# Performance work log

Hardware: AMD Instinct MI355X
Metric: run time of the kernel (lower is better)

## Reference

```python
import jax, jax.numpy as jnp
import numpy as np

B, N, D = 4, 1024, 512
H = 8
HD = D // H  # 64
EPS = 1e-12  # F.normalize eps


def _l2_normalize(t):
    # torch.nn.functional.normalize(p=2, dim=-1): x / max(||x||_2, eps)
    nrm = jnp.sqrt(jnp.sum(t * t, axis=-1, keepdims=True))
    return t / jnp.maximum(nrm, EPS)


def setup_inputs() -> dict:
    key = jax.random.key(0)
    ks = jax.random.split(key, 5)
    scale = 1.0 / np.sqrt(D)
    inp = {
        "x": jax.random.normal(ks[0], (B, N, D), dtype=jnp.float32),
        "Wq": jax.random.normal(ks[1], (D, D), dtype=jnp.float32) * scale,
        "Wk": jax.random.normal(ks[2], (D, D), dtype=jnp.float32) * scale,
        "Wv": jax.random.normal(ks[3], (D, D), dtype=jnp.float32) * scale,
        "Wo": jax.random.normal(ks[4], (D, D), dtype=jnp.float32) * scale,
        "bq": jnp.zeros((D,), dtype=jnp.float32),
        "bk": jnp.zeros((D,), dtype=jnp.float32),
        "bv": jnp.zeros((D,), dtype=jnp.float32),
        "bo": jnp.zeros((D,), dtype=jnp.float32),
    }
    return inp


def reference(x, Wq, Wk, Wv, Wo, bq, bk, bv, bo):
    b, n, d = x.shape
    # projections (nn.Linear: x @ W.T + b), split heads -> (b, h, n, hd)
    def split_heads(t):
        return t.reshape(b, n, H, HD).transpose(0, 2, 1, 3)

    q = split_heads(x @ Wq.T + bq)
    k = split_heads(x @ Wk.T + bk)
    v = split_heads(x @ Wv.T + bv)

    q = _l2_normalize(jax.nn.elu(q))
    k = _l2_normalize(jax.nn.elu(k))

    # causal linear attention: running prefix sum of k (outer) v states
    kv_step = jnp.einsum('bhnd,bhne->bhnde', k, v)      # (b,h,n,hd,hd)
    kv_prefix = jnp.cumsum(kv_step, axis=2)             # causal prefix state
    out = jnp.einsum('bhnd,bhnde->bhne', q, kv_prefix)  # (b,h,n,hd)

    out = out.transpose(0, 2, 1, 3).reshape(b, n, d)
    return out @ Wo.T + bo
```

## Files before the change

kernel.cpp:

```cpp
#include <hip/hip_runtime.h>
#include <cmath>

#define BB 4
#define NN 1024
#define DD 512
#define HH 8
#define HDIM 64
#define ROWS (BB * NN)
#define NCHUNK 16
#define KA 512
#define WMAT ((size_t)512 * 512)

typedef _Float16 f16;
typedef f16   f16x8 __attribute__((ext_vector_type(8)));
typedef f16   f16x4 __attribute__((ext_vector_type(4)));
typedef float f32x4 __attribute__((ext_vector_type(4)));

#define GLOAD_LDS16(g, l) \
    __builtin_amdgcn_global_load_lds((const __attribute__((address_space(1))) void*)(g), \
                                     (__attribute__((address_space(3))) void*)(l), 16, 0, 0)

__global__ __launch_bounds__(256)
void split_all(const float* __restrict__ x,
               const float* __restrict__ Wq, const float* __restrict__ Wk,
               const float* __restrict__ Wv, const float* __restrict__ Wo,
               f16* __restrict__ xa, f16* __restrict__ wa)
{
    const int bid = blockIdx.x;
    const float* src;
    f16* dstbase;
    int t;
    if (bid < 2048) {
        t = bid * 256 + threadIdx.x;
        src = x;
        dstbase = xa;
    } else {
        int wb = bid - 2048;
        int m  = wb >> 8;
        t = (wb & 255) * 256 + threadIdx.x;
        src = (m == 0) ? Wq : (m == 1) ? Wk : (m == 2) ? Wv : Wo;
        dstbase = wa + (size_t)m * WMAT;
    }
    float4 v = ((const float4*)src)[t];
    int r = t >> 7;
    int c = (t & 127) * 4;
    f16x4 h;
    h[0] = (f16)v.x; h[1] = (f16)v.y; h[2] = (f16)v.z; h[3] = (f16)v.w;
    *(f16x4*)(dstbase + (size_t)r * 512 + c) = h;
}

template<int OUTMODE>
__global__ __launch_bounds__(256)
void mm_f16(const f16* __restrict__ A, const f16* __restrict__ Wm,
            const float* __restrict__ b0, const float* __restrict__ b1,
            const float* __restrict__ b2,
            f16* __restrict__ qf, f16* __restrict__ kf,
            f16* __restrict__ ktb, f16* __restrict__ vtb,
            float* __restrict__ obase)
{
    constexpr int BN = (OUTMODE == 0) ? 128 : 64;
    constexpr int NW = BN / 32;
    constexpr int BR = BN / 32;

    __shared__ __align__(16) f16 As[128 * 64];
    __shared__ __align__(16) f16 Bs[BN * 64];

    const int t    = threadIdx.x;
    const int lane = t & 63;
    const int wid  = t >> 6;
    const int wr   = wid >> 1;
    const int wc   = wid & 1;
    const int l16  = lane & 15;
    const int g16  = lane >> 4;

    const int nwg = 32 * gridDim.y;
    const int lin = blockIdx.y * 32 + blockIdx.x;
    const int swz = (lin & 7) * (nwg >> 3) + (lin >> 3);
    const int bx  = swz & 31;
    const int by  = swz >> 5;

    const int r0 = bx * 128;
    const int c0 = by * BN;
    const int z  = (OUTMODE == 0) ? (c0 >> 9) : 0;
    const int cw = (OUTMODE == 0) ? (c0 & 511) : c0;

    const f16* Wz = Wm + (size_t)z * WMAT;

    f32x4 acc[4][NW] = {};

    for (int kt = 0; kt < 8; ++kt) {
        const int kb = kt * 64;
        #pragma unroll
        for (int i = 0; i < 4; ++i) {
            int f = i * 256 + t;
            int row = f >> 3;
            int sc  = (f & 7) ^ (row & 7);
            GLOAD_LDS16(A + (size_t)(r0 + row) * KA + kb + sc * 8, As + f * 8);
        }
        #pragma unroll
        for (int i = 0; i < BR; ++i) {
            int f = i * 256 + t;
            int row = f >> 3;
            int sc  = (f & 7) ^ (row & 7);
            GLOAD_LDS16(Wz + (size_t)(cw + row) * KA + kb + sc * 8, Bs + f * 8);
        }
        __syncthreads();

        #pragma unroll
        for (int kk = 0; kk < 2; ++kk) {
            f16x8 af[4], bfr[NW];
            #pragma unroll
            for (int mi = 0; mi < 4; ++mi) {
                int lr = wr * 64 + mi * 16 + l16;
                int sc = (kk * 4 + g16) ^ (lr & 7);
                af[mi] = *(const f16x8*)(As + lr * 64 + sc * 8);
            }
            #pragma unroll
            for (int ni = 0; ni < NW; ++ni) {
                int lr = wc * (BN / 2) + ni * 16 + l16;
                int sc = (kk * 4 + g16) ^ (lr & 7);
                bfr[ni] = *(const f16x8*)(Bs + lr * 64 + sc * 8);
            }
            #pragma unroll
            for (int mi = 0; mi < 4; ++mi)
                #pragma unroll
                for (int ni = 0; ni < NW; ++ni)
                    acc[mi][ni] = __builtin_amdgcn_mfma_f32_16x16x32_f16(af[mi], bfr[ni], acc[mi][ni], 0, 0, 0);
        }
        __syncthreads();
    }

    if (OUTMODE == 1) {
        #pragma unroll
        for (int mi = 0; mi < 4; ++mi)
            #pragma unroll
            for (int ni = 0; ni < NW; ++ni) {
                int cg = c0 + wc * (BN / 2) + ni * 16 + l16;
                float bv = b0[cg];
                #pragma unroll
                for (int r = 0; r < 4; ++r) {
                    int rg = r0 + wr * 64 + mi * 16 + g16 * 4 + r;
                    obase[(size_t)rg * DD + cg] = acc[mi][ni][r] + bv;
                }
            }
    } else {
        const float* bias = (z == 0) ? b0 : (z == 1) ? b1 : b2;

        #pragma unroll
        for (int mi = 0; mi < 4; ++mi)
            #pragma unroll
            for (int ni = 0; ni < NW; ++ni) {
                float bv = bias[cw + wc * 64 + ni * 16 + l16];
                #pragma unroll
                for (int r = 0; r < 4; ++r) {
                    float v = acc[mi][ni][r] + bv;
                    if (z < 2) v = (v > 0.f) ? v : expm1f(v);
                    acc[mi][ni][r] = v;
                }
            }
        if (z < 2) {
            #pragma unroll
            for (int mi = 0; mi < 4; ++mi)
                #pragma unroll
                for (int r = 0; r < 4; ++r) {
                    float ss = 0.f;
                    #pragma unroll
                    for (int ni = 0; ni < NW; ++ni) ss += acc[mi][ni][r] * acc[mi][ni][r];
                    ss += __shfl_xor(ss, 1);
                    ss += __shfl_xor(ss, 2);
                    ss += __shfl_xor(ss, 4);
                    ss += __shfl_xor(ss, 8);
                    float sc = 1.f / fmaxf(sqrtf(ss), 1e-12f);
                    #pragma unroll
                    for (int ni = 0; ni < NW; ++ni) acc[mi][ni][r] *= sc;
                }
        }

        const int h = (cw >> 6) + wc;
        const int b = r0 >> 10;

        if (z <= 1) {
            f16* plane = (z == 0) ? qf : kf;
            #pragma unroll
            for (int mi = 0; mi < 4; ++mi)
                #pragma unroll
                for (int r = 0; r < 4; ++r) {
                    int rg = r0 + wr * 64 + mi * 16 + g16 * 4 + r;
                    f16* dst = plane + ((size_t)(b * HH + h) * NN + (rg & 1023)) * HDIM;
                    #pragma unroll
                    for (int ni = 0; ni < NW; ++ni) dst[ni * 16 + l16] = (f16)acc[mi][ni][r];
                }
        }

        if (z >= 1) {
            f16* tb = (z == 1) ? ktb : vtb;
            f16* T = (wid < 2) ? (As + wid * 4096) : (Bs + (wid - 2) * 4096);
            #pragma unroll
            for (int mi = 0; mi < 4; ++mi)
                #pragma unroll
                for (int ni = 0; ni < NW; ++ni)
                    #pragma unroll
                    for (int r = 0; r < 4; ++r) {
                        int n_ = mi * 16 + g16 * 4 + r;
                        int d_ = ni * 16 + l16;
                        *(f16*)((char*)T + d_ * 128 + (((n_ >> 3) ^ (d_ & 7)) * 16) + (n_ & 7) * 2)
                            = (f16)acc[mi][ni][r];
                    }
            __syncthreads();
            const int n0 = (r0 & 1023) + wr * 64;
            #pragma unroll
            for (int p = 0; p < 8; ++p) {
                int d_ = p * 8 + (lane >> 3);
                int ck = lane & 7;
                f16x8 v8 = *(const f16x8*)((char*)T + d_ * 128 + ((ck ^ (d_ & 7)) * 16));
                *(f16x8*)(tb + ((size_t)(b * HH + h) * HDIM + d_) * NN + n0 + ck * 8) = v8;
            }
        }
    }
}

__global__ __launch_bounds__(256)
void chunk_state(const f16* __restrict__ ktb, const f16* __restrict__ vtb,
                 float* __restrict__ S)
{
    __shared__ __align__(16) f16 Kt[64 * 64];
    __shared__ __align__(16) f16 Vt[64 * 64];

    const int bh = blockIdx.x;
    const int ch = blockIdx.y;
    const int t  = threadIdx.x;
    const int lane = t & 63;
    const int wid  = t >> 6;
    const int wr   = wid >> 1;
    const int wc   = wid & 1;
    const int l16  = lane & 15;
    const int g16  = lane >> 4;

    #pragma unroll
    for (int i = 0; i < 2; ++i) {
        int f = i * 256 + t;
        int row = f >> 3;
        int sc  = (f & 7) ^ (row & 7);
        GLOAD_LDS16(ktb + ((size_t)bh * HDIM + row) * NN + ch * 64 + sc * 8, Kt + f * 8);
        GLOAD_LDS16(vtb + ((size_t)bh * HDIM + row) * NN + ch * 64 + sc * 8, Vt + f * 8);
    }
    __syncthreads();

    f32x4 acc[2][2] = {};
    #pragma unroll
    for (int ks = 0; ks < 2; ++ks) {
        f16x8 af[2], bfr[2];
        #pragma unroll
        for (int mi = 0; mi < 2; ++mi) {
            int row = wr * 32 + mi * 16 + l16;
            int sc  = (ks * 4 + g16) ^ (row & 7);
            af[mi] = *(const f16x8*)(Vt + row * 64 + sc * 8);
        }
        #pragma unroll
        for (int ni = 0; ni < 2; ++ni) {
            int row = wc * 32 + ni * 16 + l16;
            int sc  = (ks * 4 + g16) ^ (row & 7);
            bfr[ni] = *(const f16x8*)(Kt + row * 64 + sc * 8);
        }
        #pragma unroll
        for (int mi = 0; mi < 2; ++mi)
            #pragma unroll
            for (int ni = 0; ni < 2; ++ni)
                acc[mi][ni] = __builtin_amdgcn_mfma_f32_16x16x32_f16(af[mi], bfr[ni], acc[mi][ni], 0, 0, 0);
    }

    float* sg = S + ((size_t)bh * NCHUNK + ch) * 4096;
    #pragma unroll
    for (int mi = 0; mi < 2; ++mi)
        #pragma unroll
        for (int ni = 0; ni < 2; ++ni)
            #pragma unroll
            for (int r = 0; r < 4; ++r) {
                int e = wr * 32 + mi * 16 + g16 * 4 + r;
                int d = wc * 32 + ni * 16 + l16;
                sg[e * 64 + d] = acc[mi][ni][r];
            }
}

__global__ __launch_bounds__(256)
void attn_chunk(const f16* __restrict__ qf, const f16* __restrict__ kf,
                const f16* __restrict__ vtb, const float* __restrict__ S,
                f16* __restrict__ aug)
{
    __shared__ __align__(16) f16 Qs[64 * 64];
    __shared__ __align__(16) f16 Ks[64 * 64];
    __shared__ __align__(16) f16 Vt[64 * 64];
    __shared__ __align__(16) f16 Pt[64 * 64];
    __shared__ __align__(16) f16 Ss[64 * 64];

    const int bh = blockIdx.x;
    const int ch = blockIdx.y;
    const int t  = threadIdx.x;
    const int lane = t & 63;
    const int wid  = t >> 6;
    const int wr   = wid >> 1;
    const int wc   = wid & 1;
    const int l16  = lane & 15;
    const int g16  = lane >> 4;

    #pragma unroll
    for (int i = 0; i < 2; ++i) {
        int f = i * 256 + t;
        int row = f >> 3;
        int sc  = (f & 7) ^ (row & 7);
        GLOAD_LDS16(qf  + ((size_t)bh * NN + ch * 64 + row) * HDIM + sc * 8, Qs + f * 8);
        GLOAD_LDS16(kf  + ((size_t)bh * NN + ch * 64 + row) * HDIM + sc * 8, Ks + f * 8);
        GLOAD_LDS16(vtb + ((size_t)bh * HDIM + row) * NN + ch * 64 + sc * 8, Vt + f * 8);
    }

    {
        f32x4 r4[4] = {};
        const float* stb = S + (size_t)bh * NCHUNK * 4096;
        for (int c = 0; c < ch; ++c) {
            const f32x4* p = (const f32x4*)(stb + (size_t)c * 4096 + t * 16);
            #pragma unroll
            for (int j = 0; j < 4; ++j) r4[j] += p[j];
        }
        const int e  = t >> 2;
        const int d0 = (t & 3) * 16;
        f16x8 h0, h1;
        #pragma unroll
        for (int j = 0; j < 8; ++j) { h0[j] = (f16)r4[j >> 2][j & 3]; h1[j] = (f16)r4[2 + (j >> 2)][j & 3]; }
        int s0 = (d0 >> 3);
        *(f16x8*)((char*)Pt + e * 128 + ((s0 ^ (e & 7)) * 16))       = h0;
        *(f16x8*)((char*)Pt + e * 128 + (((s0 + 1) ^ (e & 7)) * 16)) = h1;
    }
    __syncthreads();

    f32x4 sacc[2][2] = {};
    #pragma unroll
    for (int ks = 0; ks < 2; ++ks) {
        f16x8 af[2], bfr[2];
        #pragma unroll
        for (int mi = 0; mi < 2; ++mi) {
            int row = wr * 32 + mi * 16 + l16;
            int sc  = (ks * 4 + g16) ^ (row & 7);
            af[mi] = *(const f16x8*)(Qs + row * 64 + sc * 8);
        }
        #pragma unroll
        for (int ni = 0; ni < 2; ++ni) {
            int row = wc * 32 + ni * 16 + l16;
            int sc  = (ks * 4 + g16) ^ (row & 7);
            bfr[ni] = *(const f16x8*)(Ks + row * 64 + sc * 8);
        }
        #pragma unroll
        for (int mi = 0; mi < 2; ++mi)
            #pragma unroll
            for (int ni = 0; ni < 2; ++ni)
                sacc[mi][ni] = __builtin_amdgcn_mfma_f32_16x16x32_f16(af[mi], bfr[ni], sacc[mi][ni], 0, 0, 0);
    }
    #pragma unroll
    for (int mi = 0; mi < 2; ++mi)
        #pragma unroll
        for (int ni = 0; ni < 2; ++ni)
            #pragma unroll
            for (int r = 0; r < 4; ++r) {
                int i = wr * 32 + mi * 16 + g16 * 4 + r;
                int j = wc * 32 + ni * 16 + l16;
                float v = (j <= i) ? sacc[mi][ni][r] : 0.f;
                *(f16*)((char*)Ss + i * 128 + (((j >> 3) ^ (i & 7)) * 16) + (j & 7) * 2) = (f16)v;
            }
    __syncthreads();

    f32x4 oacc[2][2] = {};
    #pragma unroll
    for (int ks = 0; ks < 2; ++ks) {
        f16x8 af[2], bfr[2];
        #pragma unroll
        for (int mi = 0; mi < 2; ++mi) {
            int row = wr * 32 + mi * 16 + l16;
            int sc  = (ks * 4 + g16) ^ (row & 7);
            af[mi] = *(const f16x8*)(Qs + row * 64 + sc * 8);
        }
        #pragma unroll
        for (int ni = 0; ni < 2; ++ni) {
            int row = wc * 32 + ni * 16 + l16;
            int sc  = (ks * 4 + g16) ^ (row & 7);
            bfr[ni] = *(const f16x8*)(Pt + row * 64 + sc * 8);
        }
        #pragma unroll
        for (int mi = 0; mi < 2; ++mi)
            #pragma unroll
            for (int ni = 0; ni < 2; ++ni)
                oacc[mi][ni] = __builtin_amdgcn_mfma_f32_16x16x32_f16(af[mi], bfr[ni], oacc[mi][ni], 0, 0, 0);
    }
    #pragma unroll
    for (int ks = 0; ks < 2; ++ks) {
        f16x8 af[2], bfr[2];
        #pragma unroll
        for (int mi = 0; mi < 2; ++mi) {
            int row = wr * 32 + mi * 16 + l16;
            int sc  = (ks * 4 + g16) ^ (row & 7);
            af[mi] = *(const f16x8*)(Ss + row * 64 + sc * 8);
        }
        #pragma unroll
        for (int ni = 0; ni < 2; ++ni) {
            int row = wc * 32 + ni * 16 + l16;
            int sc  = (ks * 4 + g16) ^ (row & 7);
            bfr[ni] = *(const f16x8*)(Vt + row * 64 + sc * 8);
        }
        #pragma unroll
        for (int mi = 0; mi < 2; ++mi)
            #pragma unroll
            for (int ni = 0; ni < 2; ++ni)
                oacc[mi][ni] = __builtin_amdgcn_mfma_f32_16x16x32_f16(af[mi], bfr[ni], oacc[mi][ni], 0, 0, 0);
    }

    const int b = bh >> 3;
    const int h = bh & 7;
    #pragma unroll
    for (int mi = 0; mi < 2; ++mi)
        #pragma unroll
        for (int ni = 0; ni < 2; ++ni)
            #pragma unroll
            for (int r = 0; r < 4; ++r) {
                int i = wr * 32 + mi * 16 + g16 * 4 + r;
                int e = wc * 32 + ni * 16 + l16;
                aug[((size_t)(b * NN + ch * 64 + i)) * KA + h * HDIM + e] = (f16)oacc[mi][ni][r];
            }
}

extern "C" void kernel_launch(void* const* d_in, const int* in_sizes, int n_in,
                              void* d_out, int out_size, void* d_ws, size_t ws_size,
                              hipStream_t stream)
{
    (void)in_sizes; (void)n_in; (void)out_size; (void)ws_size;

    const float* x  = (const float*)d_in[0];
    const float* Wq = (const float*)d_in[1];
    const float* Wk = (const float*)d_in[2];
    const float* Wv = (const float*)d_in[3];
    const float* Wo = (const float*)d_in[4];
    const float* bq = (const float*)d_in[5];
    const float* bk = (const float*)d_in[6];
    const float* bv = (const float*)d_in[7];
    const float* bo = (const float*)d_in[8];
    float* out = (float*)d_out;

    char* ws = (char*)d_ws;
    f16*   qf  = (f16*)  (ws);
    f16*   kf  = (f16*)  (ws + (size_t)4  * 1024 * 1024);
    f16*   ktb = (f16*)  (ws + (size_t)8  * 1024 * 1024);
    f16*   vtb = (f16*)  (ws + (size_t)12 * 1024 * 1024);
    float* st  = (float*)(ws + (size_t)16 * 1024 * 1024);
    f16*   xa  = (f16*)  (ws + (size_t)24 * 1024 * 1024);
    f16*   aug = (f16*)  (ws + (size_t)28 * 1024 * 1024);
    f16*   wa  = (f16*)  (ws + (size_t)32 * 1024 * 1024);

    dim3 blk(256);

    split_all<<<dim3(3072), blk, 0, stream>>>(x, Wq, Wk, Wv, Wo, xa, wa);

    mm_f16<0><<<dim3(32, 12), blk, 0, stream>>>(xa, wa, bq, bk, bv, qf, kf, ktb, vtb, nullptr);

    chunk_state<<<dim3(32, NCHUNK), blk, 0, stream>>>(ktb, vtb, st);
    attn_chunk<<<dim3(32, NCHUNK), blk, 0, stream>>>(qf, kf, vtb, st, aug);

    mm_f16<1><<<dim3(32, 8), blk, 0, stream>>>(aug, wa + (size_t)3 * WMAT, bo, nullptr, nullptr,
                                               nullptr, nullptr, nullptr, nullptr, out);
}
```

Measured before the change: 60.28 us.

## Compute per-chunk exclusive state prefix in a sequential pipelined kernel

Replaces the per-chunk state kernel plus the quadratic prefix re-summation in the attention kernel with a new kernel. It walks the chunks in order with double-buffered async loads, keeps a running fp16-converted exclusive prefix, and writes ready-to-use prefix tiles. The attention kernel then loads its prefix tile directly instead of summing up to 15 fp32 state tiles. This removes redundant global reads and fp32 traffic, but the prefix computation becomes a serial loop over 16 chunks on only 128 blocks, which limits parallelism.

```diff
diff --git a/kernel.cpp b/kernel.cpp
--- a/kernel.cpp
+++ b/kernel.cpp
@@ -220,11 +220,84 @@
 }
 
 __global__ __launch_bounds__(256)
-void chunk_state(const f16* __restrict__ ktb, const f16* __restrict__ vtb,
-                 float* __restrict__ S)
+void state_prefix(const f16* __restrict__ ktb, const f16* __restrict__ vtb,
+                  f16* __restrict__ ptb)
 {
-    __shared__ __align__(16) f16 Kt[64 * 64];
+    __shared__ __align__(16) f16 Kt[2][64 * 64];
+    __shared__ __align__(16) f16 Vt[2][64 * 64];
+    __shared__ __align__(16) f16 PtL[16 * 64];
+
+    const int bh = blockIdx.x;
+    const int eq = blockIdx.y;
+    const int t  = threadIdx.x;
+    const int lane = t & 63;
+    const int wid  = t >> 6;
+    const int l16  = lane & 15;
+    const int g16  = lane >> 4;
+
+    auto stage = [&](int ch, int buf) {
+        #pragma unroll
+        for (int i = 0; i < 2; ++i) {
+            int f = i * 256 + t;
+            int row = f >> 3;
+            int sc  = (f & 7) ^ (row & 7);
+            GLOAD_LDS16(ktb + ((size_t)bh * HDIM + row) * NN + ch * 64 + sc * 8, Kt[buf] + f * 8);
+            GLOAD_LDS16(vtb + ((size_t)bh * HDIM + row) * NN + ch * 64 + sc * 8, Vt[buf] + f * 8);
+        }
+    };
+
+    float pref[4] = {};
+    const int d = wid * 16 + l16;
+
+    stage(0, 0);
+
+    for (int ch = 0; ch < NCHUNK; ++ch) {
+        const int buf = ch & 1;
+        stage(ch < 15 ? ch + 1 : 15, buf ^ 1);
+
+        #pragma unroll
+        for (int r = 0; r < 4; ++r) {
+            int e = g16 * 4 + r;
+            *(f16*)((char*)PtL + e * 128 + (((d >> 3) ^ (e & 7)) * 16) + (d & 7) * 2)
+                = (f16)pref[r];
+        }
+
+        asm volatile("s_waitcnt vmcnt(4)" ::: "memory");
+        asm volatile("s_waitcnt lgkmcnt(0)" ::: "memory");
+        __builtin_amdgcn_s_barrier();
+        __builtin_amdgcn_sched_barrier(0);
+
+        {
+            f16x4 v4 = *(const f16x4*)(PtL + t * 4);
+            *(f16x4*)(ptb + (size_t)(bh * NCHUNK + ch) * 4096 + eq * 1024 + t * 4) = v4;
+        }
+
+        f32x4 sacc = {};
+        #pragma unroll
+        for (int ks = 0; ks < 2; ++ks) {
+            int ra = eq * 16 + l16;
+            f16x8 av = *(const f16x8*)(Vt[buf] + ra * 64 + ((ks * 4 + g16) ^ (ra & 7)) * 8);
+            int rb = wid * 16 + l16;
+            f16x8 bv = *(const f16x8*)(Kt[buf] + rb * 64 + ((ks * 4 + g16) ^ (rb & 7)) * 8);
+            sacc = __builtin_amdgcn_mfma_f32_16x16x32_f16(av, bv, sacc, 0, 0, 0);
+        }
+        #pragma unroll
+        for (int r = 0; r < 4; ++r) pref[r] += sacc[r];
+
+        __builtin_amdgcn_s_barrier();
+    }
+}
+
+__global__ __launch_bounds__(256)
+void attn_chunk(const f16* __restrict__ qf, const f16* __restrict__ kf,
+                const f16* __restrict__ vtb, const f16* __restrict__ ptb,
+                f16* __restrict__ aug)
+{
+    __shared__ __align__(16) f16 Qs[64 * 64];
+    __shared__ __align__(16) f16 Ks[64 * 64];
     __shared__ __align__(16) f16 Vt[64 * 64];
+    __shared__ __align__(16) f16 Pt[64 * 64];
+    __shared__ __align__(16) f16 Ss[64 * 64];
 
     const int bh = blockIdx.x;
     const int ch = blockIdx.y;
@@ -241,94 +314,10 @@
         int f = i * 256 + t;
         int row = f >> 3;
         int sc  = (f & 7) ^ (row & 7);
-        GLOAD_LDS16(ktb + ((size_t)bh * HDIM + row) * NN + ch * 64 + sc * 8, Kt + f * 8);
-        GLOAD_LDS16(vtb + ((size_t)bh * HDIM + row) * NN + ch * 64 + sc * 8, Vt + f * 8);
-    }
-    __syncthreads();
-
-    f32x4 acc[2][2] = {};
-    #pragma unroll
-    for (int ks = 0; ks < 2; ++ks) {
-        f16x8 af[2], bfr[2];
-        #pragma unroll
-        for (int mi = 0; mi < 2; ++mi) {
-            int row = wr * 32 + mi * 16 + l16;
-            int sc  = (ks * 4 + g16) ^ (row & 7);
-            af[mi] = *(const f16x8*)(Vt + row * 64 + sc * 8);
-        }
-        #pragma unroll
-        for (int ni = 0; ni < 2; ++ni) {
-            int row = wc * 32 + ni * 16 + l16;
-            int sc  = (ks * 4 + g16) ^ (row & 7);
-            bfr[ni] = *(const f16x8*)(Kt + row * 64 + sc * 8);
-        }
-        #pragma unroll
-        for (int mi = 0; mi < 2; ++mi)
-            #pragma unroll
-            for (int ni = 0; ni < 2; ++ni)
-                acc[mi][ni] = __builtin_amdgcn_mfma_f32_16x16x32_f16(af[mi], bfr[ni], acc[mi][ni], 0, 0, 0);
-    }
-
-    float* sg = S + ((size_t)bh * NCHUNK + ch) * 4096;
-    #pragma unroll
-    for (int mi = 0; mi < 2; ++mi)
-        #pragma unroll
-        for (int ni = 0; ni < 2; ++ni)
-            #pragma unroll
-            for (int r = 0; r < 4; ++r) {
-                int e = wr * 32 + mi * 16 + g16 * 4 + r;
-                int d = wc * 32 + ni * 16 + l16;
-                sg[e * 64 + d] = acc[mi][ni][r];
-            }
-}
-
-__global__ __launch_bounds__(256)
-void attn_chunk(const f16* __restrict__ qf, const f16* __restrict__ kf,
-                const f16* __restrict__ vtb, const float* __restrict__ S,
-                f16* __restrict__ aug)
-{
-    __shared__ __align__(16) f16 Qs[64 * 64];
-    __shared__ __align__(16) f16 Ks[64 * 64];
-    __shared__ __align__(16) f16 Vt[64 * 64];
-    __shared__ __align__(16) f16 Pt[64 * 64];
-    __shared__ __align__(16) f16 Ss[64 * 64];
-
-    const int bh = blockIdx.x;
-    const int ch = blockIdx.y;
-    const int t  = threadIdx.x;
-    const int lane = t & 63;
-    const int wid  = t >> 6;
-    const int wr   = wid >> 1;
-    const int wc   = wid & 1;
-    const int l16  = lane & 15;
-    const int g16  = lane >> 4;
-
-    #pragma unroll
-    for (int i = 0; i < 2; ++i) {
-        int f = i * 256 + t;
-        int row = f >> 3;
-        int sc  = (f & 7) ^ (row & 7);
         GLOAD_LDS16(qf  + ((size_t)bh * NN + ch * 64 + row) * HDIM + sc * 8, Qs + f * 8);
         GLOAD_LDS16(kf  + ((size_t)bh * NN + ch * 64 + row) * HDIM + sc * 8, Ks + f * 8);
         GLOAD_LDS16(vtb + ((size_t)bh * HDIM + row) * NN + ch * 64 + sc * 8, Vt + f * 8);
-    }
-
-    {
-        f32x4 r4[4] = {};
-        const float* stb = S + (size_t)bh * NCHUNK * 4096;
-        for (int c = 0; c < ch; ++c) {
-            const f32x4* p = (const f32x4*)(stb + (size_t)c * 4096 + t * 16);
-            #pragma unroll
-            for (int j = 0; j < 4; ++j) r4[j] += p[j];
-        }
-        const int e  = t >> 2;
-        const int d0 = (t & 3) * 16;
-        f16x8 h0, h1;
-        #pragma unroll
-        for (int j = 0; j < 8; ++j) { h0[j] = (f16)r4[j >> 2][j & 3]; h1[j] = (f16)r4[2 + (j >> 2)][j & 3]; }
-        int s0 = (d0 >> 3);
-        *(f16x8*)((char*)Pt + e * 128 + ((s0 ^ (e & 7)) * 16))       = h0;
-        *(f16x8*)((char*)Pt + e * 128 + (((s0 + 1) ^ (e & 7)) * 16)) = h1;
+        GLOAD_LDS16(ptb + (size_t)(bh * NCHUNK + ch) * 4096 + f * 8, Pt + f * 8);
     }
     __syncthreads();
 
@@ -443,14 +432,14 @@
     float* out = (float*)d_out;
 
     char* ws = (char*)d_ws;
-    f16*   qf  = (f16*)  (ws);
-    f16*   kf  = (f16*)  (ws + (size_t)4  * 1024 * 1024);
-    f16*   ktb = (f16*)  (ws + (size_t)8  * 1024 * 1024);
-    f16*   vtb = (f16*)  (ws + (size_t)12 * 1024 * 1024);
-    float* st  = (float*)(ws + (size_t)16 * 1024 * 1024);
-    f16*   xa  = (f16*)  (ws + (size_t)24 * 1024 * 1024);
-    f16*   aug = (f16*)  (ws + (size_t)28 * 1024 * 1024);
-    f16*   wa  = (f16*)  (ws + (size_t)32 * 1024 * 1024);
+    f16* qf  = (f16*)(ws);
+    f16* kf  = (f16*)(ws + (size_t)4  * 1024 * 1024);
+    f16* ktb = (f16*)(ws + (size_t)8  * 1024 * 1024);
+    f16* vtb = (f16*)(ws + (size_t)12 * 1024 * 1024);
+    f16* ptb = (f16*)(ws + (size_t)16 * 1024 * 1024);
+    f16* xa  = (f16*)(ws + (size_t)20 * 1024 * 1024);
+    f16* aug = (f16*)(ws + (size_t)24 * 1024 * 1024);
+    f16* wa  = (f16*)(ws + (size_t)28 * 1024 * 1024);
 
     dim3 blk(256);
 
@@ -458,8 +447,8 @@
 
     mm_f16<0><<<dim3(32, 12), blk, 0, stream>>>(xa, wa, bq, bk, bv, qf, kf, ktb, vtb, nullptr);
 
-    chunk_state<<<dim3(32, NCHUNK), blk, 0, stream>>>(ktb, vtb, st);
-    attn_chunk<<<dim3(32, NCHUNK), blk, 0, stream>>>(qf, kf, vtb, st, aug);
+    state_prefix<<<dim3(32, 4), blk, 0, stream>>>(ktb, vtb, ptb);
+    attn_chunk<<<dim3(32, NCHUNK), blk, 0, stream>>>(qf, kf, vtb, ptb, aug);
 
     mm_f16<1><<<dim3(32, 8), blk, 0, stream>>>(aug, wa + (size_t)3 * WMAT, bo, nullptr, nullptr,
                                                nullptr, nullptr, nullptr, nullptr, out);
```

Result: no change. 60.46 us (+0.3%).
